# Kernel tuning notes

Hardware: AMD Instinct MI355X
Metric: run time of the kernel (lower is better)

## Reference

```python
import jax, jax.numpy as jnp
import numpy as np

N_NODES = 50000
N_EDGES = 625000
IN_DIM = 128
OUT_DIM = 128


def setup_inputs() -> dict:
    key = jax.random.key(0)
    ks = jax.random.split(key, 8)
    feats = jax.random.normal(ks[0], (N_NODES, IN_DIM), dtype=jnp.float32)
    src = jax.random.randint(ks[1], (N_EDGES,), 0, N_NODES, dtype=jnp.int64)
    dst = jax.random.randint(ks[2], (N_EDGES,), 0, N_NODES, dtype=jnp.int64)
    # nn.Linear default init: U(-1/sqrt(fan_in), 1/sqrt(fan_in))
    bf = 1.0 / np.sqrt(IN_DIM)
    W_f = jax.random.uniform(ks[3], (OUT_DIM, IN_DIM), jnp.float32, -bf, bf)
    b_f = jax.random.uniform(ks[4], (OUT_DIM,), jnp.float32, -bf, bf)
    bp = 1.0 / np.sqrt(OUT_DIM)
    W_phy = jax.random.uniform(ks[5], (OUT_DIM, OUT_DIM), jnp.float32, -bp, bp)
    b_phy = jax.random.uniform(ks[6], (OUT_DIM,), jnp.float32, -bp, bp)
    eps = jnp.zeros((1,), dtype=jnp.float32)  # init_eps = 0
    return {"feats": feats, "src": src, "dst": dst, "W_f": W_f, "b_f": b_f,
            "W_phy": W_phy, "b_phy": b_phy, "eps": eps}


def reference(feats, src, dst, W_f, b_f, W_phy, b_phy, eps):
    # mlp_f (num_mlps=1): linear + relu
    h = jax.nn.relu(feats @ W_f.T + b_f)              # [N, out_dim]
    # update_all(copy_u('h'), sum): sum messages h[src] at dst
    n = jax.ops.segment_sum(h[src], dst, num_segments=N_NODES)  # [N, out_dim]
    # faithful to source: h = 1 + eps * h + n
    h = 1.0 + eps * h + n
    # mlp_phy (num_mlps=1): linear + relu
    h = jax.nn.relu(h @ W_phy.T + b_phy)
    return h
```

## Files before the change

kernel.cpp:

```cpp
#include <hip/hip_runtime.h>

#define N_NODES 50000
#define N_EDGES 625000
#define DIM 128
#define CAP 64

typedef __bf16 bf16x8 __attribute__((ext_vector_type(8)));
typedef __bf16 bf16x4 __attribute__((ext_vector_type(4)));
typedef __bf16 bf16x2 __attribute__((ext_vector_type(2)));
typedef float f32x4 __attribute__((ext_vector_type(4)));

__device__ __forceinline__ float bflo(unsigned u) { return __uint_as_float(u << 16); }
__device__ __forceinline__ float bfhi(unsigned u) { return __uint_as_float(u & 0xffff0000u); }

__global__ __launch_bounds__(512) void gemm1_fill_k(
    const float* __restrict__ A_f32,
    const float* __restrict__ W,
    const float* __restrict__ bias,
    __bf16* __restrict__ out_bf16,
    const int* __restrict__ src,
    const int* __restrict__ dst,
    int* __restrict__ cnt,
    int* __restrict__ bucket,
    const float* __restrict__ W_phy,
    __bf16* __restrict__ Wb,
    int gemm_blocks)
{
    const int t = threadIdx.x;

    if ((int)blockIdx.x >= gemm_blocks) {
        if ((int)blockIdx.x == gemm_blocks) {
            if (t < 16) {
                bf16x8 z = {};
                *(bf16x8*)&out_bf16[(size_t)N_NODES * DIM + t * 8] = z;
            }
            for (int i = t; i < 4096; i += 512) {
                float4 f = ((const float4*)W_phy)[i];
                bf16x4 pk = { (__bf16)f.x, (__bf16)f.y, (__bf16)f.z, (__bf16)f.w };
                *(bf16x4*)&Wb[i * 4] = pk;
            }
        }
        int idx = ((int)blockIdx.x - gemm_blocks) * 512 + t;
        if (idx < N_EDGES / 4) {
            int4 s4 = ((const int4*)src)[idx];
            int4 d4 = ((const int4*)dst)[idx];
            int p0 = atomicAdd(&cnt[d4.x], 1);
            bucket[(d4.x << 6) + p0] = s4.x;
            int p1 = atomicAdd(&cnt[d4.y], 1);
            bucket[(d4.y << 6) + p1] = s4.y;
            int p2 = atomicAdd(&cnt[d4.z], 1);
            bucket[(d4.z << 6) + p2] = s4.z;
            int p3 = atomicAdd(&cnt[d4.w], 1);
            bucket[(d4.w << 6) + p3] = s4.w;
        }
        return;
    }

    __shared__ __align__(16) __bf16 w_lds[128 * 136];

    for (int i = t; i < 4096; i += 512) {
        float4 f = ((const float4*)W)[i];
        int n = i >> 5;
        int k = (i & 31) << 2;
        bf16x4 pk = { (__bf16)f.x, (__bf16)f.y, (__bf16)f.z, (__bf16)f.w };
        *(bf16x4*)&w_lds[n * 136 + k] = pk;
    }
    __syncthreads();

    const int wave = t >> 6;
    const int lane = t & 63;
    const int q = lane >> 4;
    const int mr = lane & 15;

    const int m0 = blockIdx.x * 128 + wave * 16;
    int arow = m0 + mr;
    if (arow >= N_NODES) arow = N_NODES - 1;

    f32x4 acc[8] = {};

#pragma unroll
    for (int ks = 0; ks < 4; ++ks) {
        const int k0 = ks * 32 + q * 8;
        const float4* ap = (const float4*)&A_f32[(size_t)arow * DIM + k0];
        float4 a0 = ap[0], a1 = ap[1];
        bf16x8 af;
        af[0] = (__bf16)a0.x; af[1] = (__bf16)a0.y;
        af[2] = (__bf16)a0.z; af[3] = (__bf16)a0.w;
        af[4] = (__bf16)a1.x; af[5] = (__bf16)a1.y;
        af[6] = (__bf16)a1.z; af[7] = (__bf16)a1.w;
#pragma unroll
        for (int nt = 0; nt < 8; ++nt) {
            bf16x8 bfr = *(const bf16x8*)&w_lds[(nt * 16 + mr) * 136 + k0];
            acc[nt] = __builtin_amdgcn_mfma_f32_16x16x32_bf16(af, bfr, acc[nt], 0, 0, 0);
        }
    }

    __syncthreads();
    float* lds_f = (float*)w_lds;
    const int nb = blockIdx.x * 128;

#pragma unroll
    for (int half = 0; half < 2; ++half) {
        if ((wave >> 2) == half) {
            int lw = wave & 3;
#pragma unroll
            for (int nt = 0; nt < 8; ++nt)
#pragma unroll
                for (int r = 0; r < 4; ++r)
                    lds_f[(lw * 16 + q * 4 + r) * 132 + nt * 16 + mr] = acc[nt][r];
        }
        __syncthreads();
        for (int i = t; i < 2048; i += 512) {
            int lr = i >> 5;
            int cg = (i & 31) << 2;
            int grow = nb + half * 64 + lr;
            if (grow < N_NODES) {
                float4 v = *(const float4*)&lds_f[lr * 132 + cg];
                float4 b4 = *(const float4*)&bias[cg];
                bf16x4 o;
                o[0] = (__bf16)fmaxf(v.x + b4.x, 0.f);
                o[1] = (__bf16)fmaxf(v.y + b4.y, 0.f);
                o[2] = (__bf16)fmaxf(v.z + b4.z, 0.f);
                o[3] = (__bf16)fmaxf(v.w + b4.w, 0.f);
                *(bf16x4*)&out_bf16[(size_t)grow * DIM + cg] = o;
            }
        }
        __syncthreads();
    }
}

__global__ __launch_bounds__(256) void agg_combine_k(
    const __bf16* __restrict__ h,
    const int* __restrict__ cnt,
    const int* __restrict__ bucket,
    const float* __restrict__ eps_p,
    __bf16* __restrict__ c)
{
    const int t = threadIdx.x;
    const int node = blockIdx.x * 4 + (t >> 6);
    const int lane = t & 63;
    const int ch = lane << 1;

    const int deg = cnt[node];
    const int base = node << 6;
    const int ZROW = N_NODES;

    float ax = 0.f, ay = 0.f;
    for (int e = 0; e < deg; e += 4) {
        uint4 i4 = *(const uint4*)&bucket[base + e];
        int s0 = (int)i4.x;
        int s1 = (e + 1 < deg) ? (int)i4.y : ZROW;
        int s2 = (e + 2 < deg) ? (int)i4.z : ZROW;
        int s3 = (e + 3 < deg) ? (int)i4.w : ZROW;
        unsigned v0 = *(const unsigned*)&h[(size_t)s0 * DIM + ch];
        unsigned v1 = *(const unsigned*)&h[(size_t)s1 * DIM + ch];
        unsigned v2 = *(const unsigned*)&h[(size_t)s2 * DIM + ch];
        unsigned v3 = *(const unsigned*)&h[(size_t)s3 * DIM + ch];
        ax += bflo(v0) + bflo(v1) + bflo(v2) + bflo(v3);
        ay += bfhi(v0) + bfhi(v1) + bfhi(v2) + bfhi(v3);
    }

    const float eps = eps_p[0];
    unsigned sv = *(const unsigned*)&h[(size_t)node * DIM + ch];
    bf16x2 o;
    o[0] = (__bf16)(1.0f + eps * bflo(sv) + ax);
    o[1] = (__bf16)(1.0f + eps * bfhi(sv) + ay);
    *(bf16x2*)&c[(size_t)node * DIM + ch] = o;
}

__global__ __launch_bounds__(512) void gemm2_k(
    const __bf16* __restrict__ A,
    const __bf16* __restrict__ Wb,
    const float* __restrict__ bias,
    float* __restrict__ out)
{
    __shared__ __align__(16) __bf16 w_lds[128 * 136];

    const int t = threadIdx.x;

    for (int i = t; i < 2048; i += 512) {
        int n = i >> 4;
        int kk = (i & 15) << 3;
        bf16x8 v = *(const bf16x8*)&Wb[n * DIM + kk];
        *(bf16x8*)&w_lds[n * 136 + kk] = v;
    }
    __syncthreads();

    const int wave = t >> 6;
    const int lane = t & 63;
    const int q = lane >> 4;
    const int mr = lane & 15;

    const int m0 = blockIdx.x * 128 + wave * 16;
    int arow = m0 + mr;
    if (arow >= N_NODES) arow = N_NODES - 1;

    f32x4 acc[8] = {};

#pragma unroll
    for (int ks = 0; ks < 4; ++ks) {
        const int k0 = ks * 32 + q * 8;
        bf16x8 af = *(const bf16x8*)&A[(size_t)arow * DIM + k0];
#pragma unroll
        for (int nt = 0; nt < 8; ++nt) {
            bf16x8 bfr = *(const bf16x8*)&w_lds[(nt * 16 + mr) * 136 + k0];
            acc[nt] = __builtin_amdgcn_mfma_f32_16x16x32_bf16(af, bfr, acc[nt], 0, 0, 0);
        }
    }

    __syncthreads();
    float* lds_f = (float*)w_lds;
    const int nb = blockIdx.x * 128;

#pragma unroll
    for (int half = 0; half < 2; ++half) {
        if ((wave >> 2) == half) {
            int lw = wave & 3;
#pragma unroll
            for (int nt = 0; nt < 8; ++nt)
#pragma unroll
                for (int r = 0; r < 4; ++r)
                    lds_f[(lw * 16 + q * 4 + r) * 132 + nt * 16 + mr] = acc[nt][r];
        }
        __syncthreads();
        for (int i = t; i < 2048; i += 512) {
            int lr = i >> 5;
            int cg = (i & 31) << 2;
            int grow = nb + half * 64 + lr;
            if (grow < N_NODES) {
                float4 v = *(const float4*)&lds_f[lr * 132 + cg];
                float4 b4 = *(const float4*)&bias[cg];
                v.x = fmaxf(v.x + b4.x, 0.f);
                v.y = fmaxf(v.y + b4.y, 0.f);
                v.z = fmaxf(v.z + b4.z, 0.f);
                v.w = fmaxf(v.w + b4.w, 0.f);
                *(float4*)&out[(size_t)grow * DIM + cg] = v;
            }
        }
        __syncthreads();
    }
}

extern "C" void kernel_launch(void* const* d_in, const int* in_sizes, int n_in,
                              void* d_out, int out_size, void* d_ws, size_t ws_size,
                              hipStream_t stream) {
    const float* feats = (const float*)d_in[0];
    const int*   src   = (const int*)d_in[1];
    const int*   dst   = (const int*)d_in[2];
    const float* W_f   = (const float*)d_in[3];
    const float* b_f   = (const float*)d_in[4];
    const float* W_phy = (const float*)d_in[5];
    const float* b_phy = (const float*)d_in[6];
    const float* eps   = (const float*)d_in[7];
    float* out = (float*)d_out;

    const size_t HN = (size_t)(N_NODES + 1) * DIM;
    __bf16* h   = (__bf16*)d_ws;
    __bf16* c   = h + HN;
    int* bucket = (int*)(c + (size_t)N_NODES * DIM);
    int* cnt    = bucket + (size_t)N_NODES * CAP;
    __bf16* Wb  = (__bf16*)(cnt + N_NODES);

    const int gblocks = (N_NODES + 127) / 128;
    const int fblocks = (N_EDGES / 4 + 511) / 512;

    hipMemsetAsync(cnt, 0, N_NODES * sizeof(int), stream);

    gemm1_fill_k<<<gblocks + fblocks, 512, 0, stream>>>(
        feats, W_f, b_f, h, src, dst, cnt, bucket, W_phy, Wb, gblocks);

    agg_combine_k<<<N_NODES / 4, 256, 0, stream>>>(
        h, cnt, bucket, eps, c);

    gemm2_k<<<gblocks, 512, 0, stream>>>(
        c, Wb, b_phy, out);
}
```

Measured before the change: 158.6 us.

## Fuse neighbor aggregation into second GEMM via LDS-staged combined rows

Merges the aggregation/combine kernel into the second GEMM kernel. Each wave aggregates 16 nodes and writes the combined bf16 rows into shared memory, which then feed the MFMA loop directly. This removes the intermediate global buffer round-trip and one kernel launch. Neighbor indices are loaded once per lane and broadcast with readlane, and the gather is unrolled by 8. The cost is that the gather now runs with only 391 blocks of 512 threads, so there is less parallelism to hide gather latency, and LDS use per block doubles.

New measurement: 155.0 us. -2.2%, faster.

```diff
diff --git a/kernel.cpp b/kernel.cpp
--- a/kernel.cpp
+++ b/kernel.cpp
@@ -129,52 +129,18 @@
     }
 }
 
-__global__ __launch_bounds__(256) void agg_combine_k(
+__global__ __launch_bounds__(512, 4) void agg_gemm2_k(
     const __bf16* __restrict__ h,
     const int* __restrict__ cnt,
     const int* __restrict__ bucket,
     const float* __restrict__ eps_p,
-    __bf16* __restrict__ c)
-{
-    const int t = threadIdx.x;
-    const int node = blockIdx.x * 4 + (t >> 6);
-    const int lane = t & 63;
-    const int ch = lane << 1;
-
-    const int deg = cnt[node];
-    const int base = node << 6;
-    const int ZROW = N_NODES;
-
-    float ax = 0.f, ay = 0.f;
-    for (int e = 0; e < deg; e += 4) {
-        uint4 i4 = *(const uint4*)&bucket[base + e];
-        int s0 = (int)i4.x;
-        int s1 = (e + 1 < deg) ? (int)i4.y : ZROW;
-        int s2 = (e + 2 < deg) ? (int)i4.z : ZROW;
-        int s3 = (e + 3 < deg) ? (int)i4.w : ZROW;
-        unsigned v0 = *(const unsigned*)&h[(size_t)s0 * DIM + ch];
-        unsigned v1 = *(const unsigned*)&h[(size_t)s1 * DIM + ch];
-        unsigned v2 = *(const unsigned*)&h[(size_t)s2 * DIM + ch];
-        unsigned v3 = *(const unsigned*)&h[(size_t)s3 * DIM + ch];
-        ax += bflo(v0) + bflo(v1) + bflo(v2) + bflo(v3);
-        ay += bfhi(v0) + bfhi(v1) + bfhi(v2) + bfhi(v3);
-    }
-
-    const float eps = eps_p[0];
-    unsigned sv = *(const unsigned*)&h[(size_t)node * DIM + ch];
-    bf16x2 o;
-    o[0] = (__bf16)(1.0f + eps * bflo(sv) + ax);
-    o[1] = (__bf16)(1.0f + eps * bfhi(sv) + ay);
-    *(bf16x2*)&c[(size_t)node * DIM + ch] = o;
-}
-
-__global__ __launch_bounds__(512) void gemm2_k(
-    const __bf16* __restrict__ A,
     const __bf16* __restrict__ Wb,
     const float* __restrict__ bias,
     float* __restrict__ out)
 {
-    __shared__ __align__(16) __bf16 w_lds[128 * 136];
+    __shared__ __align__(16) __bf16 lds[2 * 128 * 136];
+    __bf16* const w_lds = lds;
+    __bf16* const a_lds = lds + 128 * 136;
 
     const int t = threadIdx.x;
 
@@ -184,23 +150,70 @@
         bf16x8 v = *(const bf16x8*)&Wb[n * DIM + kk];
         *(bf16x8*)&w_lds[n * 136 + kk] = v;
     }
-    __syncthreads();
 
     const int wave = t >> 6;
     const int lane = t & 63;
+    const int ch = lane << 1;
+    const int rowbase = __builtin_amdgcn_readfirstlane(blockIdx.x * 128 + wave * 16);
+    const float eps = eps_p[0];
+
+    int degv[16];
+    int idxv[16];
+#pragma unroll
+    for (int i = 0; i < 16; ++i) {
+        const int node = rowbase + i;
+        const bool ok = node < N_NODES;
+        degv[i] = ok ? cnt[node] : 0;
+        idxv[i] = ok ? bucket[(node << 6) | lane] : N_NODES;
+    }
+
+#pragma unroll
+    for (int i = 0; i < 16; ++i) {
+        const int node = rowbase + i;
+        const int nd = (node < N_NODES) ? node : N_NODES;
+        const int deg = degv[i];
+        const unsigned sv = *(const unsigned*)&h[(size_t)nd * DIM + ch];
+        const int s = (lane < deg) ? idxv[i] : N_NODES;
+        float ax = 0.f, ay = 0.f;
+        for (int e = 0; e < deg; e += 8) {
+            int s0 = __builtin_amdgcn_readlane(s, e + 0);
+            int s1 = __builtin_amdgcn_readlane(s, e + 1);
+            int s2 = __builtin_amdgcn_readlane(s, e + 2);
+            int s3 = __builtin_amdgcn_readlane(s, e + 3);
+            int s4 = __builtin_amdgcn_readlane(s, e + 4);
+            int s5 = __builtin_amdgcn_readlane(s, e + 5);
+            int s6 = __builtin_amdgcn_readlane(s, e + 6);
+            int s7 = __builtin_amdgcn_readlane(s, e + 7);
+            unsigned v0 = *(const unsigned*)&h[(size_t)s0 * DIM + ch];
+            unsigned v1 = *(const unsigned*)&h[(size_t)s1 * DIM + ch];
+            unsigned v2 = *(const unsigned*)&h[(size_t)s2 * DIM + ch];
+            unsigned v3 = *(const unsigned*)&h[(size_t)s3 * DIM + ch];
+            unsigned v4 = *(const unsigned*)&h[(size_t)s4 * DIM + ch];
+            unsigned v5 = *(const unsigned*)&h[(size_t)s5 * DIM + ch];
+            unsigned v6 = *(const unsigned*)&h[(size_t)s6 * DIM + ch];
+            unsigned v7 = *(const unsigned*)&h[(size_t)s7 * DIM + ch];
+            ax += (bflo(v0) + bflo(v1)) + (bflo(v2) + bflo(v3))
+                + (bflo(v4) + bflo(v5)) + (bflo(v6) + bflo(v7));
+            ay += (bfhi(v0) + bfhi(v1)) + (bfhi(v2) + bfhi(v3))
+                + (bfhi(v4) + bfhi(v5)) + (bfhi(v6) + bfhi(v7));
+        }
+        ax = 1.0f + eps * bflo(sv) + ax;
+        ay = 1.0f + eps * bfhi(sv) + ay;
+        bf16x2 o; o[0] = (__bf16)ax; o[1] = (__bf16)ay;
+        *(bf16x2*)&a_lds[(wave * 16 + i) * 136 + ch] = o;
+    }
+
+    __syncthreads();
+
     const int q = lane >> 4;
     const int mr = lane & 15;
 
-    const int m0 = blockIdx.x * 128 + wave * 16;
-    int arow = m0 + mr;
-    if (arow >= N_NODES) arow = N_NODES - 1;
-
     f32x4 acc[8] = {};
 
 #pragma unroll
     for (int ks = 0; ks < 4; ++ks) {
         const int k0 = ks * 32 + q * 8;
-        bf16x8 af = *(const bf16x8*)&A[(size_t)arow * DIM + k0];
+        bf16x8 af = *(const bf16x8*)&a_lds[(wave * 16 + mr) * 136 + k0];
 #pragma unroll
         for (int nt = 0; nt < 8; ++nt) {
             bf16x8 bfr = *(const bf16x8*)&w_lds[(nt * 16 + mr) * 136 + k0];
@@ -209,7 +222,7 @@
     }
 
     __syncthreads();
-    float* lds_f = (float*)w_lds;
+    float* lds_f = (float*)lds;
     const int nb = blockIdx.x * 128;
 
 #pragma unroll
@@ -223,9 +236,9 @@
                     lds_f[(lw * 16 + q * 4 + r) * 132 + nt * 16 + mr] = acc[nt][r];
         }
         __syncthreads();
-        for (int i = t; i < 2048; i += 512) {
-            int lr = i >> 5;
-            int cg = (i & 31) << 2;
+        for (int i2 = t; i2 < 2048; i2 += 512) {
+            int lr = i2 >> 5;
+            int cg = (i2 & 31) << 2;
             int grow = nb + half * 64 + lr;
             if (grow < N_NODES) {
                 float4 v = *(const float4*)&lds_f[lr * 132 + cg];
@@ -256,8 +269,7 @@
 
     const size_t HN = (size_t)(N_NODES + 1) * DIM;
     __bf16* h   = (__bf16*)d_ws;
-    __bf16* c   = h + HN;
-    int* bucket = (int*)(c + (size_t)N_NODES * DIM);
+    int* bucket = (int*)(h + HN);
     int* cnt    = bucket + (size_t)N_NODES * CAP;
     __bf16* Wb  = (__bf16*)(cnt + N_NODES);
 
@@ -269,9 +281,6 @@
     gemm1_fill_k<<<gblocks + fblocks, 512, 0, stream>>>(
         feats, W_f, b_f, h, src, dst, cnt, bucket, W_phy, Wb, gblocks);
 
-    agg_combine_k<<<N_NODES / 4, 256, 0, stream>>>(
-        h, cnt, bucket, eps, c);
-
-    gemm2_k<<<gblocks, 512, 0, stream>>>(
-        c, Wb, b_phy, out);
+    agg_gemm2_k<<<gblocks, 512, 0, stream>>>(
+        h, cnt, bucket, eps, Wb, b_phy, out);
 }
```
